# Kernel optimization log

Measured on AMD Instinct MI355X. Metric: run time of the kernel, lower is better.

Reference implementation:

```python
import math
import jax, jax.numpy as jnp
import numpy as np

EPS = 1e-7
TOPK = 10
FACTOR_IOU = 6.0
FACTOR_CLS = 0.5


def ciou(b1, b2):
    """Complete IoU. b1, b2 broadcastable [..., 4] boxes (x1,y1,x2,y2)."""
    xi1 = jnp.maximum(b1[..., 0], b2[..., 0])
    yi1 = jnp.maximum(b1[..., 1], b2[..., 1])
    xi2 = jnp.minimum(b1[..., 2], b2[..., 2])
    yi2 = jnp.minimum(b1[..., 3], b2[..., 3])
    inter = jnp.clip(xi2 - xi1, 0) * jnp.clip(yi2 - yi1, 0)
    a1 = (b1[..., 2] - b1[..., 0]) * (b1[..., 3] - b1[..., 1])
    a2 = (b2[..., 2] - b2[..., 0]) * (b2[..., 3] - b2[..., 1])
    union = a1 + a2 - inter
    iou = inter / (union + EPS)
    cx1 = (b1[..., 2] + b1[..., 0]) * 0.5
    cy1 = (b1[..., 3] + b1[..., 1]) * 0.5
    cx2 = (b2[..., 2] + b2[..., 0]) * 0.5
    cy2 = (b2[..., 3] + b2[..., 1]) * 0.5
    cent = (cx1 - cx2) ** 2 + (cy1 - cy2) ** 2
    cw = jnp.maximum(b1[..., 2], b2[..., 2]) - jnp.minimum(b1[..., 0], b2[..., 0])
    ch = jnp.maximum(b1[..., 3], b2[..., 3]) - jnp.minimum(b1[..., 1], b2[..., 1])
    diag = cw ** 2 + ch ** 2 + EPS
    diou = iou - cent / diag
    arctan = (jnp.arctan((b1[..., 2] - b1[..., 0]) / (b1[..., 3] - b1[..., 1] + EPS))
              - jnp.arctan((b2[..., 2] - b2[..., 0]) / (b2[..., 3] - b2[..., 1] + EPS)))
    v = (4.0 / math.pi ** 2) * arctan ** 2
    alpha = jax.lax.stop_gradient(v / (v - iou + 1.0 + EPS))
    return diou - alpha * v


def box_matcher(target, predict_cls, predict_bbox, anchors, class_num):
    """target [B,T,5]; predict_cls [B,A,C] logits; predict_bbox [B,A,4]; anchors [A,2].
    Returns anchor_matched_targets [B,A,C+4], valid_mask [B,A] bool."""
    B, T = target.shape[0], target.shape[1]
    A = anchors.shape[0]
    tcls = jnp.clip(target[..., 0].astype(jnp.int32), 0)        # [B,T]
    tbox = target[..., 1:5]                                       # [B,T,4]

    # grid mask: anchor center inside target box
    ax = anchors[None, None, :, 0]
    ay = anchors[None, None, :, 1]
    grid_mask = ((tbox[:, :, None, 0] < ax) & (ax < tbox[:, :, None, 2])
                 & (tbox[:, :, None, 1] < ay) & (ay < tbox[:, :, None, 3]))  # [B,T,A]

    # pairwise CIoU target x anchor
    iou_mat = jnp.clip(ciou(tbox[:, :, None, :], predict_bbox[:, None, :, :]), 0.0, 1.0)  # [B,T,A]

    # class prob of each target's class at each anchor
    pc = jax.nn.sigmoid(predict_cls)                              # [B,A,C]
    idx_bta = jnp.broadcast_to(tcls[:, :, None], (B, T, A))
    cls_mat = jnp.take_along_axis(pc.transpose(0, 2, 1), idx_bta, axis=1)  # [B,T,A]

    target_matrix = grid_mask * iou_mat ** FACTOR_IOU * cls_mat ** FACTOR_CLS

    # top-k targets per anchor (topk over anchor axis, as in source)
    vals, idx = jax.lax.top_k(target_matrix, TOPK)                # [B,T,K]
    bi = jnp.arange(B)[:, None, None]
    ti = jnp.arange(T)[None, :, None]
    topk_targets = jnp.zeros_like(target_matrix).at[bi, ti, idx].set(vals)
    topk_mask = (topk_targets > 0).astype(jnp.int32)              # [B,T,A]

    # resolve anchors assigned to multiple targets by max IoU
    duplicates = (topk_mask.sum(1, keepdims=True) > 1)            # [B,1,A]
    max_idx = jax.nn.one_hot(jnp.argmax(iou_mat, axis=1), T, dtype=jnp.int32).transpose(0, 2, 1)  # [B,T,A]
    topk_mask = jnp.where(duplicates, max_idx, topk_mask)
    unique_indices = jnp.argmax(topk_mask, axis=1)                # [B,A]
    valid = topk_mask.sum(1)                                      # [B,A]

    align_bbox = jnp.take_along_axis(tbox, jnp.broadcast_to(unique_indices[:, :, None], (B, A, 4)), axis=1)  # [B,A,4]
    align_cls_idx = jnp.take_along_axis(tcls, unique_indices, axis=1)  # [B,A]
    align_cls = jax.nn.one_hot(align_cls_idx, class_num, dtype=target_matrix.dtype)  # [B,A,C]

    iou_m = iou_mat * topk_mask
    tm_m = target_matrix * topk_mask
    max_target = tm_m.max(axis=-1, keepdims=True)                 # [B,T,1]
    max_iou = iou_m.max(axis=-1, keepdims=True)                   # [B,T,1]
    normalize_term = tm_m / (max_target + 1e-9) * max_iou         # [B,T,A]
    normalize_term = jnp.take_along_axis(normalize_term.transpose(0, 2, 1),
                                         unique_indices[:, :, None], axis=2)  # [B,A,1]
    align_cls = align_cls * normalize_term * valid[:, :, None].astype(align_cls.dtype)
    anchor_matched_targets = jnp.concatenate([align_cls, align_bbox], axis=-1)
    return anchor_matched_targets, (valid > 0)


def setup_inputs() -> dict:
    key = jax.random.key(0)
    ks = jax.random.split(key, 6)
    B, T, C = 32, 64, 80
    img = 640.0
    cells = []
    for s in (8, 16, 32):
        n = 640 // s
        xs = (np.arange(n, dtype=np.float32) + 0.5) * s
        gx, gy = np.meshgrid(xs, xs)
        cells.append(np.stack([gx.ravel(), gy.ravel()], axis=1))
    anchors = jnp.asarray(np.concatenate(cells, 0), dtype=jnp.float32)  # [8400,2]
    A = anchors.shape[0]
    cls = jax.random.randint(ks[0], (B, T, 1), 0, C).astype(jnp.float32)
    cxy = jax.random.uniform(ks[1], (B, T, 2)) * img
    wh = jax.random.uniform(ks[2], (B, T, 2)) * 160.0 + 8.0
    tbox = jnp.concatenate([cxy - wh / 2, cxy + wh / 2], axis=-1)
    target = jnp.concatenate([cls, tbox], axis=-1)                # [B,T,5]
    predict_cls = jax.random.normal(ks[3], (B, A, C), dtype=jnp.float32)
    pcxy = anchors[None] + (jax.random.uniform(ks[4], (B, A, 2)) - 0.5) * 32.0
    pwh = jax.random.uniform(ks[5], (B, A, 2)) * 128.0 + 8.0
    predict_bbox = jnp.concatenate([pcxy - pwh / 2, pcxy + pwh / 2], axis=-1)  # [B,A,4]
    return {"target": target, "predict_cls": predict_cls,
            "predict_bbox": predict_bbox, "anchors": anchors}


def reference(target, predict_cls, predict_bbox, anchors):
    C = predict_cls.shape[-1]
    # matcher runs on detached predictions (as in the torch source)
    amt, valid = box_matcher(target,
                             jax.lax.stop_gradient(predict_cls),
                             jax.lax.stop_gradient(predict_bbox),
                             anchors, C)
    targets_cls = amt[..., :C]                                    # [B,A,C]
    targets_bbox = amt[..., C:]                                   # [B,A,4]
    cls_norm = jnp.maximum(targets_cls.sum(), 1.0)
    box_norm = targets_cls.sum(-1)                                # [B,A]

    # BCE-with-logits, sum / cls_norm
    x, t = predict_cls, targets_cls
    bce = jnp.maximum(x, 0) - x * t + jnp.log1p(jnp.exp(-jnp.abs(x)))
    loss_cls = bce.sum() / cls_norm

    # CIoU box loss over valid anchors (elementwise == diag of picked pairwise)
    iou_e = ciou(predict_bbox, targets_bbox)                      # [B,A]
    loss_iou = ((1.0 - iou_e) * box_norm * valid).sum() / cls_norm

    return jnp.stack([loss_iou, loss_cls])
```

## Files before the change

kernel.cpp:

```cpp
#include <hip/hip_runtime.h>
#include <climits>
#include <cmath>


#define NB 32
#define NT 64
#define NA 8400
#define NC 80
#define KTOP 10
#define NE (NT * KTOP)
#define CAP 1024
#define EPSF 1e-7f
#define INV_PI2 0.40528473456935108577f
#define LOG2E_F 1.44269504088896340736f
#define LN2_F   0.69314718055994530942f
#define BCE_BLOCKS 2048

__device__ __forceinline__ float atan_wh(float x1, float y1, float x2, float y2) {
  return atanf((x2 - x1) / (y2 - y1 + EPSF));
}

__device__ __forceinline__ float ciou_pair(
    float ax1, float ay1, float ax2, float ay2, float atA,
    float bx1, float by1, float bx2, float by2, float atB)
{
  float xi1 = fmaxf(ax1, bx1), yi1 = fmaxf(ay1, by1);
  float xi2 = fminf(ax2, bx2), yi2 = fminf(ay2, by2);
  float inter = fmaxf(xi2 - xi1, 0.f) * fmaxf(yi2 - yi1, 0.f);
  float a1 = (ax2 - ax1) * (ay2 - ay1);
  float a2 = (bx2 - bx1) * (by2 - by1);
  float iou = inter / (a1 + a2 - inter + EPSF);
  float dcx = (ax2 + ax1) * 0.5f - (bx2 + bx1) * 0.5f;
  float dcy = (ay2 + ay1) * 0.5f - (by2 + by1) * 0.5f;
  float cent = dcx * dcx + dcy * dcy;
  float cw = fmaxf(ax2, bx2) - fminf(ax1, bx1);
  float ch = fmaxf(ay2, by2) - fminf(ay1, by1);
  float diag = cw * cw + ch * ch + EPSF;
  float dv = atA - atB;
  float v = INV_PI2 * dv * dv;
  float alpha = v / (v - iou + 1.f + EPSF);
  return iou - cent / diag - alpha * v;
}

__device__ __forceinline__ float softplus_fast(float x) {
  float e = exp2f(-LOG2E_F * fabsf(x));
  float l = __log2f(1.f + e);
  return fmaxf(x, 0.f) + LN2_F * l;
}

__global__ __launch_bounds__(256) void k_bce_topk(
    const float* __restrict__ target,
    const float* __restrict__ pcls,
    const float* __restrict__ pbox,
    float* __restrict__ top_val, int* __restrict__ top_idx,
    float* __restrict__ top_iou,
    unsigned* __restrict__ mtg, unsigned* __restrict__ mig,
    double* __restrict__ bce_part, unsigned* __restrict__ ticket)
{
  int tid = threadIdx.x;
  __shared__ double red[256];

  if (blockIdx.x < BCE_BLOCKS) {
    if (blockIdx.x == 0 && tid == 0) *ticket = 0u;
    const float4* p4 = (const float4*)pcls;
    const int n4 = NB * NA * NC / 4;
    double acc = 0.0;
    for (int i = blockIdx.x * 256 + tid; i < n4; i += BCE_BLOCKS * 256) {
      float4 v = p4[i];
      float p = (softplus_fast(v.x) + softplus_fast(v.y)) +
                (softplus_fast(v.z) + softplus_fast(v.w));
      acc += (double)p;
    }
    red[tid] = acc; __syncthreads();
    for (int off = 128; off > 0; off >>= 1) {
      if (tid < off) red[tid] += red[tid + off];
      __syncthreads();
    }
    if (tid == 0) bce_part[blockIdx.x] = red[0];
    return;
  }

  int row = blockIdx.x - BCE_BLOCKS;
  if (tid == 0) { mtg[row] = 0u; mig[row] = 0u; }
  int b = row >> 6;
  const float* tg = target + (size_t)row * 5;
  float tcf = tg[0];
  float x1 = tg[1], y1 = tg[2], x2 = tg[3], y2 = tg[4];
  int tc = (int)tcf; tc = tc < 0 ? 0 : (tc > NC - 1 ? NC - 1 : tc);
  float atan_t = atan_wh(x1, y1, x2, y2);

  __shared__ int s_n;
  __shared__ float s_val[CAP];
  __shared__ int s_idx[CAP];
  __shared__ float xw_v[4];  __shared__ int xw_a[4];
  __shared__ float w_val[KTOP]; __shared__ int w_idx[KTOP];
  if (tid == 0) s_n = 0;
  __syncthreads();

  const float* pb_b = pbox + (size_t)b * NA * 4;
  const float* pc_b = pcls + (size_t)b * NA * NC;

#define LEVEL_LOOP(S, N, BASE)                                              \
  {                                                                         \
    const float s = (float)(S);                                             \
    int ix0 = (int)floorf(x1 / s - 0.5f); ix0 = ix0 < 0 ? 0 : ix0;          \
    int ix1 = (int)ceilf (x2 / s - 0.5f); ix1 = ix1 > (N)-1 ? (N)-1 : ix1;  \
    int iy0 = (int)floorf(y1 / s - 0.5f); iy0 = iy0 < 0 ? 0 : iy0;          \
    int iy1 = (int)ceilf (y2 / s - 0.5f); iy1 = iy1 > (N)-1 ? (N)-1 : iy1;  \
    int w = ix1 - ix0 + 1; w = w < 0 ? 0 : w;                               \
    int h = iy1 - iy0 + 1; h = h < 0 ? 0 : h;                               \
    int cnt = w * h;                                                        \
    for (int k = tid; k < cnt; k += 256) {                                  \
      int ix = ix0 + k % w;                                                 \
      int iy = iy0 + k / w;                                                 \
      float anx = (ix + 0.5f) * s;                                          \
      float any_ = (iy + 0.5f) * s;                                         \
      if (x1 < anx && anx < x2 && y1 < any_ && any_ < y2) {                 \
        int a = (BASE) + iy * (N) + ix;                                     \
        float4 bb = ((const float4*)pb_b)[a];                               \
        float c = ciou_pair(x1, y1, x2, y2, atan_t, bb.x, bb.y, bb.z, bb.w, \
                            atan_wh(bb.x, bb.y, bb.z, bb.w));               \
        float io = fminf(fmaxf(c, 0.f), 1.f);                               \
        float i2 = io * io;                                                 \
        float i6 = i2 * i2 * i2;                                            \
        float sc = pc_b[(size_t)a * NC + tc];                               \
        float sig = 1.f / (1.f + expf(-sc));                                \
        float tm = i6 * sqrtf(sig);                                         \
        int slot = atomicAdd(&s_n, 1);                                      \
        if (slot < CAP) { s_val[slot] = tm; s_idx[slot] = a; }              \
      }                                                                     \
    }                                                                       \
  }
  LEVEL_LOOP(8, 80, 0)
  LEVEL_LOOP(16, 40, 6400)
  LEVEL_LOOP(32, 20, 8000)
#undef LEVEL_LOOP
  __syncthreads();
  int n = s_n; if (n > CAP) n = CAP;

  float v0 = -1.f, v1 = -1.f, v2 = -1.f, v3 = -1.f;
  int a0 = INT_MAX, a1 = INT_MAX, a2 = INT_MAX, a3 = INT_MAX;
  if (tid < n)       { v0 = s_val[tid];       a0 = s_idx[tid]; }
  if (tid + 256 < n) { v1 = s_val[tid + 256]; a1 = s_idx[tid + 256]; }
  if (tid + 512 < n) { v2 = s_val[tid + 512]; a2 = s_idx[tid + 512]; }
  if (tid + 768 < n) { v3 = s_val[tid + 768]; a3 = s_idx[tid + 768]; }

  for (int k = 0; k < KTOP; k++) {
    float bv = v0; int ba = a0;
    if (v1 > bv || (v1 == bv && a1 < ba)) { bv = v1; ba = a1; }
    if (v2 > bv || (v2 == bv && a2 < ba)) { bv = v2; ba = a2; }
    if (v3 > bv || (v3 == bv && a3 < ba)) { bv = v3; ba = a3; }
#pragma unroll
    for (int off = 32; off > 0; off >>= 1) {
      float ov = __shfl_xor(bv, off); int oa = __shfl_xor(ba, off);
      if (ov > bv || (ov == bv && oa < ba)) { bv = ov; ba = oa; }
    }
    if ((tid & 63) == 0) { xw_v[tid >> 6] = bv; xw_a[tid >> 6] = ba; }
    __syncthreads();
    float fv = xw_v[0]; int fa = xw_a[0];
    { float ov = xw_v[1]; int oa = xw_a[1];
      if (ov > fv || (ov == fv && oa < fa)) { fv = ov; fa = oa; } }
    { float ov = xw_v[2]; int oa = xw_a[2];
      if (ov > fv || (ov == fv && oa < fa)) { fv = ov; fa = oa; } }
    { float ov = xw_v[3]; int oa = xw_a[3];
      if (ov > fv || (ov == fv && oa < fa)) { fv = ov; fa = oa; } }
    if (tid == 0) { w_val[k] = fv; w_idx[k] = fa; }
    if (a0 == fa) { v0 = -1.f; a0 = INT_MAX; }
    if (a1 == fa) { v1 = -1.f; a1 = INT_MAX; }
    if (a2 == fa) { v2 = -1.f; a2 = INT_MAX; }
    if (a3 == fa) { v3 = -1.f; a3 = INT_MAX; }
    __syncthreads();
  }

  if (tid < KTOP) {
    int k = tid;
    int ai = w_idx[k]; float v = w_val[k];
    float io = 0.f;
    if (ai != INT_MAX && v > 0.f) {
      float4 bb = ((const float4*)pb_b)[ai];
      float c = ciou_pair(x1, y1, x2, y2, atan_t, bb.x, bb.y, bb.z, bb.w,
                          atan_wh(bb.x, bb.y, bb.z, bb.w));
      io = fminf(fmaxf(c, 0.f), 1.f);
    } else { ai = -1; v = 0.f; }
    size_t o = (size_t)row * KTOP + k;
    top_val[o] = v; top_idx[o] = ai; top_iou[o] = io;
  }
}

__global__ __launch_bounds__(256) void k_resolve(
    const float* __restrict__ target, const float* __restrict__ pcls,
    const float* __restrict__ pbox, const float* __restrict__ anchors,
    const float* __restrict__ top_val, const int* __restrict__ top_idx,
    const float* __restrict__ top_iou,
    float* __restrict__ as_tm, float* __restrict__ as_x,
    float* __restrict__ as_cio, int* __restrict__ as_u,
    unsigned* __restrict__ mtg, unsigned* __restrict__ mig)
{
  int gid = blockIdx.x * 256 + threadIdx.x;
  int entry = gid >> 6;
  int lane = threadIdx.x & 63;
  int b = entry / NE;
  int el = entry - b * NE;

  const float* bv = top_val + (size_t)b * NE;
  const int* bix = top_idx + (size_t)b * NE;
  float v = bv[el];
  int a = bix[el];

  bool dead = (v <= 0.f);
  int cnt = 0, first = NE;
  if (!dead) {
    for (int s = lane; s < NE; s += 64) {
      float v2 = bv[s]; int a2 = bix[s];
      if (v2 > 0.f && a2 == a) { cnt++; if (s < first) first = s; }
    }
    for (int off = 32; off > 0; off >>= 1) {
      cnt += __shfl_xor(cnt, off);
      int of = __shfl_xor(first, off);
      first = of < first ? of : first;
    }
    if (first != el) dead = true;
  }
  if (dead) {
    if (lane == 0) { as_tm[entry] = 0.f; as_x[entry] = 0.f;
                     as_cio[entry] = 0.f; as_u[entry] = 0; }
    return;
  }

  const float* pb = pbox + ((size_t)b * NA + a) * 4;
  int u; float tm = -1.f, io;
  if (cnt == 1) {
    u = el / KTOP; tm = v; io = top_iou[entry];
  } else {
    const float* tg = target + (size_t)(b * NT + lane) * 5;
    float tx1 = tg[1], ty1 = tg[2], tx2 = tg[3], ty2 = tg[4];
    float ta = atan_wh(tx1, ty1, tx2, ty2);
    float bx1 = pb[0], by1 = pb[1], bx2 = pb[2], by2 = pb[3];
    float pa = atan_wh(bx1, by1, bx2, by2);
    float c = ciou_pair(tx1, ty1, tx2, ty2, ta, bx1, by1, bx2, by2, pa);
    float cc = fminf(fmaxf(c, 0.f), 1.f);
    float best = cc; int bu = lane;
    for (int off = 32; off > 0; off >>= 1) {
      float ob = __shfl_xor(best, off);
      int ou = __shfl_xor(bu, off);
      if (ob > best || (ob == best && ou < bu)) { best = ob; bu = ou; }
    }
    u = bu; io = best;
  }

  if (lane == 0) {
    const float* tgu = target + (size_t)(b * NT + u) * 5;
    float ux1 = tgu[1], uy1 = tgu[2], ux2 = tgu[3], uy2 = tgu[4];
    int cu = (int)tgu[0]; cu = cu < 0 ? 0 : (cu > NC - 1 ? NC - 1 : cu);
    float x = pcls[((size_t)b * NA + a) * NC + cu];
    if (cnt != 1) {
      float2 an = ((const float2*)anchors)[a];
      float gm = (ux1 < an.x && an.x < ux2 && uy1 < an.y && an.y < uy2) ? 1.f : 0.f;
      float i2 = io * io; float i6 = i2 * i2 * i2;
      float sig = 1.f / (1.f + expf(-x));
      tm = gm * i6 * sqrtf(sig);
    }
    float bx1 = pb[0], by1 = pb[1], bx2 = pb[2], by2 = pb[3];
    float c = ciou_pair(ux1, uy1, ux2, uy2, atan_wh(ux1, uy1, ux2, uy2),
                        bx1, by1, bx2, by2, atan_wh(bx1, by1, bx2, by2));
    as_tm[entry] = tm; as_x[entry] = x; as_cio[entry] = 1.f - c; as_u[entry] = u;
    atomicMax(&mtg[b * NT + u], __float_as_uint(tm));
    atomicMax(&mig[b * NT + u], __float_as_uint(io));
  }
}

__global__ __launch_bounds__(256) void k_sums_final(
    const float* __restrict__ as_tm, const float* __restrict__ as_x,
    const float* __restrict__ as_cio, const int* __restrict__ as_u,
    const unsigned* __restrict__ mtg, const unsigned* __restrict__ mig,
    const double* __restrict__ bce_part,
    double* __restrict__ k2_part, unsigned* __restrict__ ticket,
    float* __restrict__ out)
{
  int b = blockIdx.x;
  int tid = threadIdx.x;
  __shared__ double red[256];
  __shared__ int lastflag;

  double s1 = 0.0, s2 = 0.0, s3 = 0.0;
  for (int e = tid; e < NE; e += 256) {
    size_t o = (size_t)b * NE + e;
    float tm = as_tm[o];
    int u = as_u[o];
    float maxt = __uint_as_float(mtg[b * NT + u]);
    float maxi = __uint_as_float(mig[b * NT + u]);
    float nrm = tm / (maxt + 1e-9f) * maxi;
    s1 += (double)nrm;
    s2 += (double)as_x[o] * (double)nrm;
    s3 += (double)(as_cio[o] * nrm);
  }
  red[tid] = s1; __syncthreads();
  for (int off = 128; off > 0; off >>= 1) {
    if (tid < off) red[tid] += red[tid + off];
    __syncthreads();
  }
  if (tid == 0) k2_part[b * 3 + 0] = red[0];
  __syncthreads();
  red[tid] = s2; __syncthreads();
  for (int off = 128; off > 0; off >>= 1) {
    if (tid < off) red[tid] += red[tid + off];
    __syncthreads();
  }
  if (tid == 0) k2_part[b * 3 + 1] = red[0];
  __syncthreads();
  red[tid] = s3; __syncthreads();
  for (int off = 128; off > 0; off >>= 1) {
    if (tid < off) red[tid] += red[tid + off];
    __syncthreads();
  }
  if (tid == 0) k2_part[b * 3 + 2] = red[0];
  __syncthreads();

  if (tid == 0) {
    __threadfence();
    unsigned old = atomicAdd(ticket, 1u);
    lastflag = (old == NB - 1) ? 1 : 0;
  }
  __syncthreads();
  if (!lastflag) return;
  __threadfence();

  double s = 0.0;
  for (int i = tid; i < BCE_BLOCKS; i += 256) s += bce_part[i];
  red[tid] = s; __syncthreads();
  for (int off = 128; off > 0; off >>= 1) {
    if (tid < off) red[tid] += red[tid + off];
    __syncthreads();
  }
  double s4 = red[0]; __syncthreads();

  red[tid] = (tid < NB) ? k2_part[3 * tid + 0] : 0.0; __syncthreads();
  for (int off = 128; off > 0; off >>= 1) {
    if (tid < off) red[tid] += red[tid + off];
    __syncthreads();
  }
  double t1 = red[0]; __syncthreads();

  red[tid] = (tid < NB) ? k2_part[3 * tid + 1] : 0.0; __syncthreads();
  for (int off = 128; off > 0; off >>= 1) {
    if (tid < off) red[tid] += red[tid + off];
    __syncthreads();
  }
  double t2 = red[0]; __syncthreads();

  red[tid] = (tid < NB) ? k2_part[3 * tid + 2] : 0.0; __syncthreads();
  for (int off = 128; off > 0; off >>= 1) {
    if (tid < off) red[tid] += red[tid + off];
    __syncthreads();
  }
  double t3 = red[0];

  if (tid == 0) {
    double cn = fmax(t1, 1.0);
    out[0] = (float)(t3 / cn);
    out[1] = (float)((s4 - t2) / cn);
  }
}

extern "C" void kernel_launch(void* const* d_in, const int* in_sizes, int n_in,
                              void* d_out, int out_size, void* d_ws, size_t ws_size,
                              hipStream_t stream) {
  const float* target  = (const float*)d_in[0];
  const float* pcls    = (const float*)d_in[1];
  const float* pbox    = (const float*)d_in[2];
  const float* anchors = (const float*)d_in[3];
  float* out = (float*)d_out;

  char* ws = (char*)d_ws;
  float*    top_val = (float*)ws;
  int*      top_idx = (int*)(ws + 81920);
  float*    top_iou = (float*)(ws + 163840);
  float*    as_tm   = (float*)(ws + 245760);
  float*    as_x    = (float*)(ws + 327680);
  float*    as_cio  = (float*)(ws + 409600);
  int*      as_u    = (int*)(ws + 491520);
  unsigned* mtg     = (unsigned*)(ws + 573440);
  unsigned* mig     = (unsigned*)(ws + 581632);
  double*   k2_part = (double*)(ws + 589824);
  double*   k3_part = (double*)(ws + 590592);
  unsigned* ticket  = (unsigned*)(ws + 606976);

  k_bce_topk<<<BCE_BLOCKS + NB * NT, 256, 0, stream>>>(
      target, pcls, pbox, top_val, top_idx, top_iou, mtg, mig,
      k3_part, ticket);
  k_resolve<<<(NB * NE * 64) / 256, 256, 0, stream>>>(
      target, pcls, pbox, anchors, top_val, top_idx, top_iou,
      as_tm, as_x, as_cio, as_u, mtg, mig);
  k_sums_final<<<NB, 256, 0, stream>>>(
      as_tm, as_x, as_cio, as_u, mtg, mig, k3_part, k2_part, ticket, out);
}
```

Baseline: 80.82 us.

## Replace per-entry duplicate scan with atomic per-anchor count tables and interleave block roles

The per-entry scan over all 640 top-k entries in the resolve kernel is replaced. The top-k kernel now records, for each anchor, an atomic count of the targets that picked it and the minimum entry index. Resolve looks up these two values directly, which removes a wave-wide loop of global reads and shuffles for every entry. BCE and top-k blocks are also interleaved by block parity, so the memory-bound BCE work and the compute-heavy top-k work can share the device at the same time. The cost is a new init kernel that clears two B×A tables (about 2 MB of writes and one extra launch), plus global atomics.

```diff
diff --git a/kernel.cpp b/kernel.cpp
--- a/kernel.cpp
+++ b/kernel.cpp
@@ -48,6 +48,12 @@
   return fmaxf(x, 0.f) + LN2_F * l;
 }
 
+__global__ __launch_bounds__(256) void k_init(unsigned* __restrict__ cnt,
+                                              unsigned* __restrict__ first) {
+  int i = blockIdx.x * 256 + threadIdx.x;
+  if (i < NB * NA) { cnt[i] = 0u; first[i] = 0xFFFFFFFFu; }
+}
+
 __global__ __launch_bounds__(256) void k_bce_topk(
     const float* __restrict__ target,
     const float* __restrict__ pcls,
@@ -55,17 +61,19 @@
     float* __restrict__ top_val, int* __restrict__ top_idx,
     float* __restrict__ top_iou,
     unsigned* __restrict__ mtg, unsigned* __restrict__ mig,
+    unsigned* __restrict__ cnt_t, unsigned* __restrict__ first_t,
     double* __restrict__ bce_part, unsigned* __restrict__ ticket)
 {
   int tid = threadIdx.x;
   __shared__ double red[256];
 
-  if (blockIdx.x < BCE_BLOCKS) {
-    if (blockIdx.x == 0 && tid == 0) *ticket = 0u;
+  if (!(blockIdx.x & 1)) {
+    int vb = blockIdx.x >> 1;
+    if (vb == 0 && tid == 0) *ticket = 0u;
     const float4* p4 = (const float4*)pcls;
     const int n4 = NB * NA * NC / 4;
     double acc = 0.0;
-    for (int i = blockIdx.x * 256 + tid; i < n4; i += BCE_BLOCKS * 256) {
+    for (int i = vb * 256 + tid; i < n4; i += BCE_BLOCKS * 256) {
       float4 v = p4[i];
       float p = (softplus_fast(v.x) + softplus_fast(v.y)) +
                 (softplus_fast(v.z) + softplus_fast(v.w));
@@ -76,13 +84,14 @@
       if (tid < off) red[tid] += red[tid + off];
       __syncthreads();
     }
-    if (tid == 0) bce_part[blockIdx.x] = red[0];
+    if (tid == 0) bce_part[vb] = red[0];
     return;
   }
 
-  int row = blockIdx.x - BCE_BLOCKS;
+  int row = blockIdx.x >> 1;
   if (tid == 0) { mtg[row] = 0u; mig[row] = 0u; }
   int b = row >> 6;
+  int t = row & 63;
   const float* tg = target + (size_t)row * 5;
   float tcf = tg[0];
   float x1 = tg[1], y1 = tg[2], x2 = tg[3], y2 = tg[4];
@@ -181,6 +190,9 @@
       float c = ciou_pair(x1, y1, x2, y2, atan_t, bb.x, bb.y, bb.z, bb.w,
                           atan_wh(bb.x, bb.y, bb.z, bb.w));
       io = fminf(fmaxf(c, 0.f), 1.f);
+      unsigned el = (unsigned)(t * KTOP + k);
+      atomicAdd(&cnt_t[b * NA + ai], 1u);
+      atomicMin(&first_t[b * NA + ai], el);
     } else { ai = -1; v = 0.f; }
     size_t o = (size_t)row * KTOP + k;
     top_val[o] = v; top_idx[o] = ai; top_iou[o] = io;
@@ -192,6 +204,7 @@
     const float* __restrict__ pbox, const float* __restrict__ anchors,
     const float* __restrict__ top_val, const int* __restrict__ top_idx,
     const float* __restrict__ top_iou,
+    const unsigned* __restrict__ cnt_t, const unsigned* __restrict__ first_t,
     float* __restrict__ as_tm, float* __restrict__ as_x,
     float* __restrict__ as_cio, int* __restrict__ as_u,
     unsigned* __restrict__ mtg, unsigned* __restrict__ mig)
@@ -202,24 +215,14 @@
   int b = entry / NE;
   int el = entry - b * NE;
 
-  const float* bv = top_val + (size_t)b * NE;
-  const int* bix = top_idx + (size_t)b * NE;
-  float v = bv[el];
-  int a = bix[el];
-
-  bool dead = (v <= 0.f);
-  int cnt = 0, first = NE;
+  int a = top_idx[entry];
+  float v = top_val[entry];
+
+  bool dead = (a < 0);
+  unsigned cnt = 0;
   if (!dead) {
-    for (int s = lane; s < NE; s += 64) {
-      float v2 = bv[s]; int a2 = bix[s];
-      if (v2 > 0.f && a2 == a) { cnt++; if (s < first) first = s; }
-    }
-    for (int off = 32; off > 0; off >>= 1) {
-      cnt += __shfl_xor(cnt, off);
-      int of = __shfl_xor(first, off);
-      first = of < first ? of : first;
-    }
-    if (first != el) dead = true;
+    if (first_t[b * NA + a] != (unsigned)el) dead = true;
+    else cnt = cnt_t[b * NA + a];
   }
   if (dead) {
     if (lane == 0) { as_tm[entry] = 0.f; as_x[entry] = 0.f;
@@ -229,7 +232,7 @@
 
   const float* pb = pbox + ((size_t)b * NA + a) * 4;
   int u; float tm = -1.f, io;
-  if (cnt == 1) {
+  if (cnt == 1u) {
     u = el / KTOP; tm = v; io = top_iou[entry];
   } else {
     const float* tg = target + (size_t)(b * NT + lane) * 5;
@@ -253,7 +256,7 @@
     float ux1 = tgu[1], uy1 = tgu[2], ux2 = tgu[3], uy2 = tgu[4];
     int cu = (int)tgu[0]; cu = cu < 0 ? 0 : (cu > NC - 1 ? NC - 1 : cu);
     float x = pcls[((size_t)b * NA + a) * NC + cu];
-    if (cnt != 1) {
+    if (cnt != 1u) {
       float2 an = ((const float2*)anchors)[a];
       float gm = (ux1 < an.x && an.x < ux2 && uy1 < an.y && an.y < uy2) ? 1.f : 0.f;
       float i2 = io * io; float i6 = i2 * i2 * i2;
@@ -384,13 +387,16 @@
   double*   k2_part = (double*)(ws + 589824);
   double*   k3_part = (double*)(ws + 590592);
   unsigned* ticket  = (unsigned*)(ws + 606976);
-
-  k_bce_topk<<<BCE_BLOCKS + NB * NT, 256, 0, stream>>>(
+  unsigned* cnt_t   = (unsigned*)(ws + 607232);
+  unsigned* first_t = (unsigned*)(ws + 1682432);
+
+  k_init<<<(NB * NA + 255) / 256, 256, 0, stream>>>(cnt_t, first_t);
+  k_bce_topk<<<2 * BCE_BLOCKS, 256, 0, stream>>>(
       target, pcls, pbox, top_val, top_idx, top_iou, mtg, mig,
-      k3_part, ticket);
+      cnt_t, first_t, k3_part, ticket);
   k_resolve<<<(NB * NE * 64) / 256, 256, 0, stream>>>(
       target, pcls, pbox, anchors, top_val, top_idx, top_iou,
-      as_tm, as_x, as_cio, as_u, mtg, mig);
+      cnt_t, first_t, as_tm, as_x, as_cio, as_u, mtg, mig);
   k_sums_final<<<NB, 256, 0, stream>>>(
       as_tm, as_x, as_cio, as_u, mtg, mig, k3_part, k2_part, ticket, out);
 }
```

Result: slower. 84.30 us (+4.3%).

## Split BCE and top-k kernels; 2D row-strided gather and single-wave top-k

Applied to the files above, without the earlier changes.

Splits the fused BCE-reduction and per-target top-k kernel into two separate launches. The candidate gather now walks rows across 8 groups of 32 lanes and skips whole grid rows that fall outside the target's y-range, which removes the per-element div/mod. The top-k selection now runs in a single wavefront holding 16 candidates per lane in registers, so the per-iteration block barriers and cross-wave shared-memory merges go away. In exchange, the two kernels no longer overlap in one grid, an extra launch is added, and the register count for the candidate arrays rises.

```diff
diff --git a/kernel.cpp b/kernel.cpp
--- a/kernel.cpp
+++ b/kernel.cpp
@@ -48,40 +48,19 @@
   return fmaxf(x, 0.f) + LN2_F * l;
 }
 
-__global__ __launch_bounds__(256) void k_bce_topk(
+__global__ __launch_bounds__(256) void k_topk(
     const float* __restrict__ target,
     const float* __restrict__ pcls,
     const float* __restrict__ pbox,
     float* __restrict__ top_val, int* __restrict__ top_idx,
     float* __restrict__ top_iou,
     unsigned* __restrict__ mtg, unsigned* __restrict__ mig,
-    double* __restrict__ bce_part, unsigned* __restrict__ ticket)
+    unsigned* __restrict__ ticket)
 {
+  int row = blockIdx.x;
   int tid = threadIdx.x;
-  __shared__ double red[256];
-
-  if (blockIdx.x < BCE_BLOCKS) {
-    if (blockIdx.x == 0 && tid == 0) *ticket = 0u;
-    const float4* p4 = (const float4*)pcls;
-    const int n4 = NB * NA * NC / 4;
-    double acc = 0.0;
-    for (int i = blockIdx.x * 256 + tid; i < n4; i += BCE_BLOCKS * 256) {
-      float4 v = p4[i];
-      float p = (softplus_fast(v.x) + softplus_fast(v.y)) +
-                (softplus_fast(v.z) + softplus_fast(v.w));
-      acc += (double)p;
-    }
-    red[tid] = acc; __syncthreads();
-    for (int off = 128; off > 0; off >>= 1) {
-      if (tid < off) red[tid] += red[tid + off];
-      __syncthreads();
-    }
-    if (tid == 0) bce_part[blockIdx.x] = red[0];
-    return;
-  }
-
-  int row = blockIdx.x - BCE_BLOCKS;
   if (tid == 0) { mtg[row] = 0u; mig[row] = 0u; }
+  if (row == 0 && tid == 0) *ticket = 0u;
   int b = row >> 6;
   const float* tg = target + (size_t)row * 5;
   float tcf = tg[0];
@@ -92,42 +71,43 @@
   __shared__ int s_n;
   __shared__ float s_val[CAP];
   __shared__ int s_idx[CAP];
-  __shared__ float xw_v[4];  __shared__ int xw_a[4];
-  __shared__ float w_val[KTOP]; __shared__ int w_idx[KTOP];
   if (tid == 0) s_n = 0;
   __syncthreads();
 
   const float* pb_b = pbox + (size_t)b * NA * 4;
   const float* pc_b = pcls + (size_t)b * NA * NC;
+
+  int grp = tid >> 5;
+  int sl = tid & 31;
 
 #define LEVEL_LOOP(S, N, BASE)                                              \
   {                                                                         \
     const float s = (float)(S);                                             \
-    int ix0 = (int)floorf(x1 / s - 0.5f); ix0 = ix0 < 0 ? 0 : ix0;          \
-    int ix1 = (int)ceilf (x2 / s - 0.5f); ix1 = ix1 > (N)-1 ? (N)-1 : ix1;  \
-    int iy0 = (int)floorf(y1 / s - 0.5f); iy0 = iy0 < 0 ? 0 : iy0;          \
-    int iy1 = (int)ceilf (y2 / s - 0.5f); iy1 = iy1 > (N)-1 ? (N)-1 : iy1;  \
-    int w = ix1 - ix0 + 1; w = w < 0 ? 0 : w;                               \
-    int h = iy1 - iy0 + 1; h = h < 0 ? 0 : h;                               \
-    int cnt = w * h;                                                        \
-    for (int k = tid; k < cnt; k += 256) {                                  \
-      int ix = ix0 + k % w;                                                 \
-      int iy = iy0 + k / w;                                                 \
-      float anx = (ix + 0.5f) * s;                                          \
+    int ix0 = (int)floorf(x1 / s - 0.5f); if (ix0 < 0) ix0 = 0;             \
+    int ix1 = (int)ceilf (x2 / s - 0.5f); if (ix1 > (N)-1) ix1 = (N)-1;     \
+    int iy0 = (int)floorf(y1 / s - 0.5f); if (iy0 < 0) iy0 = 0;             \
+    int iy1 = (int)ceilf (y2 / s - 0.5f); if (iy1 > (N)-1) iy1 = (N)-1;     \
+    for (int iy = iy0 + grp; iy <= iy1; iy += 8) {                          \
       float any_ = (iy + 0.5f) * s;                                         \
-      if (x1 < anx && anx < x2 && y1 < any_ && any_ < y2) {                 \
-        int a = (BASE) + iy * (N) + ix;                                     \
-        float4 bb = ((const float4*)pb_b)[a];                               \
-        float c = ciou_pair(x1, y1, x2, y2, atan_t, bb.x, bb.y, bb.z, bb.w, \
-                            atan_wh(bb.x, bb.y, bb.z, bb.w));               \
-        float io = fminf(fmaxf(c, 0.f), 1.f);                               \
-        float i2 = io * io;                                                 \
-        float i6 = i2 * i2 * i2;                                            \
-        float sc = pc_b[(size_t)a * NC + tc];                               \
-        float sig = 1.f / (1.f + expf(-sc));                                \
-        float tm = i6 * sqrtf(sig);                                         \
-        int slot = atomicAdd(&s_n, 1);                                      \
-        if (slot < CAP) { s_val[slot] = tm; s_idx[slot] = a; }              \
+      if (y1 < any_ && any_ < y2) {                                         \
+        for (int ix = ix0 + sl; ix <= ix1; ix += 32) {                      \
+          float anx = (ix + 0.5f) * s;                                      \
+          if (x1 < anx && anx < x2) {                                       \
+            int a = (BASE) + iy * (N) + ix;                                 \
+            float4 bb = ((const float4*)pb_b)[a];                           \
+            float c = ciou_pair(x1, y1, x2, y2, atan_t,                     \
+                                bb.x, bb.y, bb.z, bb.w,                     \
+                                atan_wh(bb.x, bb.y, bb.z, bb.w));           \
+            float io = fminf(fmaxf(c, 0.f), 1.f);                           \
+            float i2 = io * io;                                             \
+            float i6 = i2 * i2 * i2;                                        \
+            float sc = pc_b[(size_t)a * NC + tc];                           \
+            float sig = 1.f / (1.f + expf(-sc));                            \
+            float tm = i6 * sqrtf(sig);                                     \
+            int slot = atomicAdd(&s_n, 1);                                  \
+            if (slot < CAP) { s_val[slot] = tm; s_idx[slot] = a; }          \
+          }                                                                 \
+        }                                                                   \
       }                                                                     \
     }                                                                       \
   }
@@ -136,45 +116,36 @@
   LEVEL_LOOP(32, 20, 8000)
 #undef LEVEL_LOOP
   __syncthreads();
+  if (tid >= 64) return;
+
   int n = s_n; if (n > CAP) n = CAP;
-
-  float v0 = -1.f, v1 = -1.f, v2 = -1.f, v3 = -1.f;
-  int a0 = INT_MAX, a1 = INT_MAX, a2 = INT_MAX, a3 = INT_MAX;
-  if (tid < n)       { v0 = s_val[tid];       a0 = s_idx[tid]; }
-  if (tid + 256 < n) { v1 = s_val[tid + 256]; a1 = s_idx[tid + 256]; }
-  if (tid + 512 < n) { v2 = s_val[tid + 512]; a2 = s_idx[tid + 512]; }
-  if (tid + 768 < n) { v3 = s_val[tid + 768]; a3 = s_idx[tid + 768]; }
-
+  int lane = tid;
+  float cv[16]; int ca[16];
+#pragma unroll
+  for (int j = 0; j < 16; j++) {
+    int e = lane + 64 * j;
+    if (e < n) { cv[j] = s_val[e]; ca[j] = s_idx[e]; }
+    else { cv[j] = -1.f; ca[j] = INT_MAX; }
+  }
+  float wv = 0.f; int wa = INT_MAX;
   for (int k = 0; k < KTOP; k++) {
-    float bv = v0; int ba = a0;
-    if (v1 > bv || (v1 == bv && a1 < ba)) { bv = v1; ba = a1; }
-    if (v2 > bv || (v2 == bv && a2 < ba)) { bv = v2; ba = a2; }
-    if (v3 > bv || (v3 == bv && a3 < ba)) { bv = v3; ba = a3; }
+    float bv = -1.f; int ba = INT_MAX;
+#pragma unroll
+    for (int j = 0; j < 16; j++)
+      if (cv[j] > bv || (cv[j] == bv && ca[j] < ba)) { bv = cv[j]; ba = ca[j]; }
 #pragma unroll
     for (int off = 32; off > 0; off >>= 1) {
       float ov = __shfl_xor(bv, off); int oa = __shfl_xor(ba, off);
       if (ov > bv || (ov == bv && oa < ba)) { bv = ov; ba = oa; }
     }
-    if ((tid & 63) == 0) { xw_v[tid >> 6] = bv; xw_a[tid >> 6] = ba; }
-    __syncthreads();
-    float fv = xw_v[0]; int fa = xw_a[0];
-    { float ov = xw_v[1]; int oa = xw_a[1];
-      if (ov > fv || (ov == fv && oa < fa)) { fv = ov; fa = oa; } }
-    { float ov = xw_v[2]; int oa = xw_a[2];
-      if (ov > fv || (ov == fv && oa < fa)) { fv = ov; fa = oa; } }
-    { float ov = xw_v[3]; int oa = xw_a[3];
-      if (ov > fv || (ov == fv && oa < fa)) { fv = ov; fa = oa; } }
-    if (tid == 0) { w_val[k] = fv; w_idx[k] = fa; }
-    if (a0 == fa) { v0 = -1.f; a0 = INT_MAX; }
-    if (a1 == fa) { v1 = -1.f; a1 = INT_MAX; }
-    if (a2 == fa) { v2 = -1.f; a2 = INT_MAX; }
-    if (a3 == fa) { v3 = -1.f; a3 = INT_MAX; }
-    __syncthreads();
-  }
-
-  if (tid < KTOP) {
-    int k = tid;
-    int ai = w_idx[k]; float v = w_val[k];
+    if (lane == k) { wv = bv; wa = ba; }
+#pragma unroll
+    for (int j = 0; j < 16; j++)
+      if (ca[j] == ba) { cv[j] = -1.f; ca[j] = INT_MAX; }
+  }
+
+  if (lane < KTOP) {
+    int ai = wa; float v = wv;
     float io = 0.f;
     if (ai != INT_MAX && v > 0.f) {
       float4 bb = ((const float4*)pb_b)[ai];
@@ -182,9 +153,29 @@
                           atan_wh(bb.x, bb.y, bb.z, bb.w));
       io = fminf(fmaxf(c, 0.f), 1.f);
     } else { ai = -1; v = 0.f; }
-    size_t o = (size_t)row * KTOP + k;
+    size_t o = (size_t)row * KTOP + lane;
     top_val[o] = v; top_idx[o] = ai; top_iou[o] = io;
   }
+}
+
+__global__ __launch_bounds__(256) void k_bce(const float* __restrict__ pcls,
+                                             double* __restrict__ part) {
+  const float4* p4 = (const float4*)pcls;
+  const int n4 = NB * NA * NC / 4;
+  double acc = 0.0;
+  for (int i = blockIdx.x * 256 + threadIdx.x; i < n4; i += BCE_BLOCKS * 256) {
+    float4 v = p4[i];
+    float p = (softplus_fast(v.x) + softplus_fast(v.y)) +
+              (softplus_fast(v.z) + softplus_fast(v.w));
+    acc += (double)p;
+  }
+  __shared__ double red[256];
+  red[threadIdx.x] = acc; __syncthreads();
+  for (int off = 128; off > 0; off >>= 1) {
+    if (threadIdx.x < off) red[threadIdx.x] += red[threadIdx.x + off];
+    __syncthreads();
+  }
+  if (threadIdx.x == 0) part[blockIdx.x] = red[0];
 }
 
 __global__ __launch_bounds__(256) void k_resolve(
@@ -385,9 +376,10 @@
   double*   k3_part = (double*)(ws + 590592);
   unsigned* ticket  = (unsigned*)(ws + 606976);
 
-  k_bce_topk<<<BCE_BLOCKS + NB * NT, 256, 0, stream>>>(
-      target, pcls, pbox, top_val, top_idx, top_iou, mtg, mig,
-      k3_part, ticket);
+  k_topk<<<NB * NT, 256, 0, stream>>>(target, pcls, pbox,
+                                      top_val, top_idx, top_iou, mtg, mig,
+                                      ticket);
+  k_bce<<<BCE_BLOCKS, 256, 0, stream>>>(pcls, k3_part);
   k_resolve<<<(NB * NE * 64) / 256, 256, 0, stream>>>(
       target, pcls, pbox, anchors, top_val, top_idx, top_iou,
       as_tm, as_x, as_cio, as_u, mtg, mig);
```

New measurement: 88.91 us. +10.0%, slower.
